# Optimization experiments

Measured on AMD Instinct MI355X. Metric: run time of the kernel, lower is better.

Reference implementation:

```python
import jax, jax.numpy as jnp
import numpy as np

D_MODEL, D_CTX, D_HEAD = 1024, 768, 16

def setup_inputs() -> dict:
    key = jax.random.key(0)
    ks = jax.random.split(key, 10)
    B, M, N = 8, 4096, 4096
    s = lambda d: 1.0 / np.sqrt(d)
    return {
        "x": jax.random.normal(ks[0], (B, M, D_MODEL), dtype=jnp.float32),
        "context": jax.random.normal(ks[1], (B, N, D_CTX), dtype=jnp.float32),
        "Wq": jax.random.uniform(ks[2], (D_MODEL, D_HEAD), jnp.float32, -s(D_MODEL), s(D_MODEL)),
        "bq": jax.random.uniform(ks[3], (D_HEAD,), jnp.float32, -s(D_MODEL), s(D_MODEL)),
        "Wk": jax.random.uniform(ks[4], (D_CTX, D_HEAD), jnp.float32, -s(D_CTX), s(D_CTX)),
        "bk": jax.random.uniform(ks[5], (D_HEAD,), jnp.float32, -s(D_CTX), s(D_CTX)),
        "Wv": jax.random.uniform(ks[6], (D_CTX, D_HEAD), jnp.float32, -s(D_CTX), s(D_CTX)),
        "bv": jax.random.uniform(ks[7], (D_HEAD,), jnp.float32, -s(D_CTX), s(D_CTX)),
        "Wo": jax.random.uniform(ks[8], (D_HEAD, D_MODEL), jnp.float32, -s(D_HEAD), s(D_HEAD)),
        "bo": jax.random.uniform(ks[9], (D_MODEL,), jnp.float32, -s(D_HEAD), s(D_HEAD)),
    }

def _kernel(t):
    # ELU+1 feature map (non-negative)
    return jax.nn.elu(t) + 1.0

def reference(x, context, Wq, bq, Wk, bk, Wv, bv, Wo, bo):
    Q = _kernel(x @ Wq + bq)            # (B, M, d_head)
    K = _kernel(context @ Wk + bk)      # (B, N, d_head)
    V = context @ Wv + bv               # (B, N, d_head)
    KtV = jnp.einsum('bnd,bne->bde', K, V)   # (B, d_head, d_head)
    num = jnp.einsum('bmd,bde->bme', Q, KtV) # (B, M, d_head)
    K_sum = K.sum(axis=1)                    # (B, d_head)
    denom = jnp.einsum('bmd,bd->bm', Q, K_sum)[..., None] + 1e-6
    out = num / denom                        # (B, M, d_head)
    return out @ Wo + bo                     # (B, M, d_model)
```

## Files before the change

### kernel.cpp

```cpp
#include <hip/hip_runtime.h>
#include <math.h>

#define B_   8
#define M_   4096
#define N_   4096
#define DM   1024
#define DC   768
#define DH   16
#define PD   8
#define KVBLOCKS (B_*N_/32)
#define CHUNKS   128

typedef float v4f __attribute__((ext_vector_type(4)));
typedef __attribute__((ext_vector_type(8))) short short8v;
typedef __attribute__((ext_vector_type(4))) float f32x4;
typedef __attribute__((ext_vector_type(4))) int int4v;

__device__ __forceinline__ float elu1(float t) {
    return t > 0.0f ? t + 1.0f : expf(t);
}
__device__ __forceinline__ float4 ld4(const float* p) { return *reinterpret_cast<const float4*>(p); }
__device__ __forceinline__ void  st4(float* p, float4 v) { *reinterpret_cast<float4*>(p) = v; }
__device__ __forceinline__ void  st4nt(float* p, float4 v) {
    v4f w; w.x = v.x; w.y = v.y; w.z = v.z; w.w = v.w;
    __builtin_nontemporal_store(w, reinterpret_cast<v4f*>(p));
}
__device__ __forceinline__ void fma4(float4& a, float s, float4 w) {
    a.x = fmaf(s, w.x, a.x); a.y = fmaf(s, w.y, a.y);
    a.z = fmaf(s, w.z, a.z); a.w = fmaf(s, w.w, a.w);
}
__device__ __forceinline__ short f2bf(float f) {
    unsigned u = __float_as_uint(f);
    unsigned r = 0x7FFFu + ((u >> 16) & 1u);
    return (short)((u + r) >> 16);
}
__device__ __forceinline__ unsigned cvtpk(float a, float b) {
    unsigned r;
    asm("v_cvt_pk_bf16_f32 %0, %1, %2" : "=v"(r) : "v"(a), "v"(b));
    return r;
}
__device__ __forceinline__ short8v mk_frag(const float4& a, const float4& b) {
    int4v iv;
    iv.x = (int)cvtpk(a.x, a.y);
    iv.y = (int)cvtpk(a.z, a.w);
    iv.z = (int)cvtpk(b.x, b.y);
    iv.w = (int)cvtpk(b.z, b.w);
    union { int4v i; short8v s; } u; u.i = iv;
    return u.s;
}

__global__ __launch_bounds__(256) void prep(
    const float* __restrict__ Wq, const float* __restrict__ Wk,
    const float* __restrict__ Wv,
    short* __restrict__ fq, short* __restrict__ fk, short* __restrict__ fv)
{
    const int id = blockIdx.x * 256 + threadIdx.x;
    if (id >= 80 * 64) return;
    const int l  = id & 63;
    const int kt = id >> 6;
    const float* W; short* dst; int ktl;
    if (kt < 32)      { W = Wq; dst = fq; ktl = kt; }
    else if (kt < 56) { W = Wk; dst = fk; ktl = kt - 32; }
    else              { W = Wv; dst = fv; ktl = kt - 56; }
    const int k0 = ktl * 32 + (l >> 4) * 8;
    const int d  = l & 15;
    short* o = dst + ((size_t)ktl * 64 + l) * 8;
    #pragma unroll
    for (int j = 0; j < 8; ++j)
        o[j] = f2bf(W[(size_t)(k0 + j) * DH + d]);
}

__global__ __launch_bounds__(256) void kvr(
    const float* __restrict__ ctx,
    const short* __restrict__ fk, const short* __restrict__ fv,
    const float* __restrict__ bk, const float* __restrict__ bv,
    float* __restrict__ part)
{
    __shared__ struct {
        float ka[2][2][16][17];
        float va[2][2][16][17];
        float sk[32][17];
        float sv[32][17];
    } sh;

    const int t  = threadIdx.x;
    const int l  = t & 63;
    const int w  = t >> 6;
    const int rt = w & 1;
    const int kh = w >> 1;
    const int g4 = l >> 4;
    const int lr = l & 15;

    float4 pa[PD], pb[PD];
    const size_t row0 = (size_t)blockIdx.x * 32;
    const float* src = ctx + (row0 + rt*16 + lr) * DC + kh*384 + g4*8;
    f32x4 accK = {0,0,0,0}, accV = {0,0,0,0};

    #pragma unroll
    for (int i = 0; i < PD; ++i) {
        pa[i] = ld4(src + i*32);
        pb[i] = ld4(src + i*32 + 4);
    }
    #pragma unroll
    for (int kt = 0; kt < 12; ++kt) {
        const int st = kt & (PD-1);
        const short8v a = mk_frag(pa[st], pb[st]);
        if (kt + PD < 12) {
            pa[st] = ld4(src + (kt+PD)*32);
            pb[st] = ld4(src + (kt+PD)*32 + 4);
        }
        const int ktg = kh*12 + kt;
        const short8v bkf = *reinterpret_cast<const short8v*>(fk + ((size_t)ktg*64 + l)*8);
        const short8v bvf = *reinterpret_cast<const short8v*>(fv + ((size_t)ktg*64 + l)*8);
        accK = __builtin_amdgcn_mfma_f32_16x16x32_bf16(a, bkf, accK, 0, 0, 0);
        accV = __builtin_amdgcn_mfma_f32_16x16x32_bf16(a, bvf, accV, 0, 0, 0);
    }

    #pragma unroll
    for (int j = 0; j < 4; ++j) {
        sh.ka[rt][kh][g4*4 + j][lr] = accK[j];
        sh.va[rt][kh][g4*4 + j][lr] = accV[j];
    }
    __syncthreads();

    #pragma unroll
    for (int i = t; i < 512; i += 256) {
        const int r = i >> 4, c = i & 15;
        const int rr = r >> 4, wr = r & 15;
        const float kk = sh.ka[rr][0][wr][c] + sh.ka[rr][1][wr][c] + bk[c];
        const float vv = sh.va[rr][0][wr][c] + sh.va[rr][1][wr][c] + bv[c];
        sh.sk[r][c] = elu1(kk);
        sh.sv[r][c] = vv;
    }
    __syncthreads();

    const int d = t >> 4, e = t & 15;
    float acc = 0.f;
    #pragma unroll 16
    for (int n = 0; n < 32; ++n) acc += sh.sk[n][d] * sh.sv[n][e];
    float* p = part + (size_t)blockIdx.x * 272;
    p[t] = acc;
    if (t < DH) {
        float ss = 0.f;
        #pragma unroll 16
        for (int n = 0; n < 32; ++n) ss += sh.sk[n][t];
        p[256 + t] = ss;
    }
}

__global__ __launch_bounds__(320) void reduce2(
    const float* __restrict__ part, float* __restrict__ comb)
{
    const int b = blockIdx.x;
    const int t = threadIdx.x;
    if (t < 272) {
        float s = 0.f;
        #pragma unroll
        for (int ch = 0; ch < CHUNKS; ++ch)
            s += part[((size_t)b*CHUNKS + ch) * 272 + t];
        comb[(size_t)b*272 + t] = s;
    }
}

__global__ __launch_bounds__(256) void qproj(
    const float* __restrict__ x,
    const short* __restrict__ fq, const float* __restrict__ bq,
    const float* __restrict__ comb,
    const float* __restrict__ Wo, const float* __restrict__ bo,
    float* __restrict__ out)
{
    __shared__ float qa[4][16][17];
    __shared__ float ql[16 * DH];
    __shared__ float ol[16 * DH];
    __shared__ float kts[272];

    const int t  = threadIdx.x;
    const int l  = t & 63;
    const int w  = t >> 6;
    const int g4 = l >> 4;
    const int lr = l & 15;
    const size_t row0 = (size_t)blockIdx.x * 16;
    const int b = blockIdx.x >> 8;

    const float* src = x + (row0 + lr) * DM + w*256 + g4*8;
    float4 pa[8], pb[8];
    #pragma unroll
    for (int i = 0; i < 8; ++i) {
        pa[i] = ld4(src + i*32);
        pb[i] = ld4(src + i*32 + 4);
    }
    if (t < 68) st4(&kts[t*4], ld4(comb + (size_t)b*272 + t*4));

    f32x4 accQ = {0,0,0,0};
    #pragma unroll
    for (int kt = 0; kt < 8; ++kt) {
        const short8v a = mk_frag(pa[kt], pb[kt]);
        const short8v bqf = *reinterpret_cast<const short8v*>(fq + ((size_t)(w*8 + kt)*64 + l)*8);
        accQ = __builtin_amdgcn_mfma_f32_16x16x32_bf16(a, bqf, accQ, 0, 0, 0);
    }
    #pragma unroll
    for (int j = 0; j < 4; ++j)
        qa[w][g4*4 + j][lr] = accQ[j];
    __syncthreads();

    {
        const int r = t >> 4, c = t & 15;
        const float v = qa[0][r][c] + qa[1][r][c] + qa[2][r][c] + qa[3][r][c] + bq[c];
        ql[r*DH + c] = elu1(v);
    }
    __syncthreads();

    if (t < 64) {
        const float* qrow = &ql[(t >> 2) * DH];
        const int jj = (t & 3) * 4;
        float den = 1e-6f;
        float4 num = make_float4(0,0,0,0);
        #pragma unroll
        for (int d4 = 0; d4 < 4; ++d4) {
            const float4 q4  = ld4(&qrow[d4*4]);
            const float4 ks4 = ld4(&kts[256 + d4*4]);
            den += q4.x*ks4.x + q4.y*ks4.y + q4.z*ks4.z + q4.w*ks4.w;
            fma4(num, q4.x, ld4(&kts[(d4*4+0)*DH + jj]));
            fma4(num, q4.y, ld4(&kts[(d4*4+1)*DH + jj]));
            fma4(num, q4.z, ld4(&kts[(d4*4+2)*DH + jj]));
            fma4(num, q4.w, ld4(&kts[(d4*4+3)*DH + jj]));
        }
        const float inv = 1.0f / den;
        float4 o4; o4.x = num.x*inv; o4.y = num.y*inv; o4.z = num.z*inv; o4.w = num.w*inv;
        st4(&ol[(t >> 2)*DH + jj], o4);
    }
    __syncthreads();

    float4 wreg[16];
    #pragma unroll
    for (int e = 0; e < 16; ++e) wreg[e] = ld4(Wo + (size_t)e*DM + t*4);
    const float4 bov = ld4(bo + t*4);

    #pragma unroll
    for (int r = 0; r < 16; ++r) {
        float4 a = bov;
        #pragma unroll
        for (int eo = 0; eo < 4; ++eo) {
            const float4 o4 = ld4(&ol[r*DH + eo*4]);
            fma4(a, o4.x, wreg[eo*4+0]); fma4(a, o4.y, wreg[eo*4+1]);
            fma4(a, o4.z, wreg[eo*4+2]); fma4(a, o4.w, wreg[eo*4+3]);
        }
        st4nt(out + (row0 + r)*DM + t*4, a);
    }
}

extern "C" void kernel_launch(void* const* d_in, const int* in_sizes, int n_in,
                              void* d_out, int out_size, void* d_ws, size_t ws_size,
                              hipStream_t stream) {
    const float* x    = (const float*)d_in[0];
    const float* ctx  = (const float*)d_in[1];
    const float* Wq   = (const float*)d_in[2];
    const float* bq   = (const float*)d_in[3];
    const float* Wk   = (const float*)d_in[4];
    const float* bk   = (const float*)d_in[5];
    const float* Wv   = (const float*)d_in[6];
    const float* bv   = (const float*)d_in[7];
    const float* Wo   = (const float*)d_in[8];
    const float* bo   = (const float*)d_in[9];
    float* out = (float*)d_out;

    float* ws = (float*)d_ws;
    float* part = ws;
    float* comb = part + (size_t)KVBLOCKS*272;
    short* fq = (short*)(comb + (size_t)B_*272);
    short* fk = fq + (size_t)32*64*8;
    short* fv = fk + (size_t)24*64*8;

    prep<<<dim3(20), dim3(256), 0, stream>>>(Wq, Wk, Wv, fq, fk, fv);
    kvr<<<dim3(KVBLOCKS), dim3(256), 0, stream>>>(ctx, fk, fv, bk, bv, part);
    reduce2<<<dim3(B_), dim3(320), 0, stream>>>(part, comb);
    qproj<<<dim3(B_*M_/16), dim3(256), 0, stream>>>(x, fq, bq, comb, Wo, bo, out);
}
```

Measured before the change: 73.49 us.

## Replace KV partial-sum reduction kernel with atomics and enlarge Q-projection row tiles

The kvr kernel now atomically accumulates its per-block KtV and K-sum partials into a zeroed per-batch buffer, so the separate reduce2 launch and the partials array go away. The qproj kernel processes 32 rows per block instead of 16. Its waves split into row-tile and K-half pairs with a register-prefetched K loop, halving the block count and amortising the Wo register load. Costs are 272 atomic adds per kvr block into only 8 small regions, a memset launch, and non-deterministic float summation order.

```diff
diff --git a/kernel.cpp b/kernel.cpp
--- a/kernel.cpp
+++ b/kernel.cpp
@@ -9,7 +9,7 @@
 #define DH   16
 #define PD   8
 #define KVBLOCKS (B_*N_/32)
-#define CHUNKS   128
+#define QBLOCKS  (B_*M_/32)
 
 typedef float v4f __attribute__((ext_vector_type(4)));
 typedef __attribute__((ext_vector_type(8))) short short8v;
@@ -74,7 +74,7 @@
     const float* __restrict__ ctx,
     const short* __restrict__ fk, const short* __restrict__ fv,
     const float* __restrict__ bk, const float* __restrict__ bv,
-    float* __restrict__ part)
+    float* __restrict__ comb)
 {
     __shared__ struct {
         float ka[2][2][16][17];
@@ -138,27 +138,13 @@
     float acc = 0.f;
     #pragma unroll 16
     for (int n = 0; n < 32; ++n) acc += sh.sk[n][d] * sh.sv[n][e];
-    float* p = part + (size_t)blockIdx.x * 272;
-    p[t] = acc;
+    float* p = comb + (size_t)(blockIdx.x >> 7) * 272;
+    atomicAdd(&p[t], acc);
     if (t < DH) {
         float ss = 0.f;
         #pragma unroll 16
         for (int n = 0; n < 32; ++n) ss += sh.sk[n][t];
-        p[256 + t] = ss;
-    }
-}
-
-__global__ __launch_bounds__(320) void reduce2(
-    const float* __restrict__ part, float* __restrict__ comb)
-{
-    const int b = blockIdx.x;
-    const int t = threadIdx.x;
-    if (t < 272) {
-        float s = 0.f;
-        #pragma unroll
-        for (int ch = 0; ch < CHUNKS; ++ch)
-            s += part[((size_t)b*CHUNKS + ch) * 272 + t];
-        comb[(size_t)b*272 + t] = s;
+        atomicAdd(&p[256 + t], ss);
     }
 }
 
@@ -169,23 +155,25 @@
     const float* __restrict__ Wo, const float* __restrict__ bo,
     float* __restrict__ out)
 {
-    __shared__ float qa[4][16][17];
-    __shared__ float ql[16 * DH];
-    __shared__ float ol[16 * DH];
+    __shared__ float qa[2][2][16][17];
+    __shared__ float ql[32 * DH];
+    __shared__ float ol[32 * DH];
     __shared__ float kts[272];
 
     const int t  = threadIdx.x;
     const int l  = t & 63;
     const int w  = t >> 6;
+    const int rt = w & 1;
+    const int kh = w >> 1;
     const int g4 = l >> 4;
     const int lr = l & 15;
-    const size_t row0 = (size_t)blockIdx.x * 16;
-    const int b = blockIdx.x >> 8;
-
-    const float* src = x + (row0 + lr) * DM + w*256 + g4*8;
-    float4 pa[8], pb[8];
-    #pragma unroll
-    for (int i = 0; i < 8; ++i) {
+    const size_t row0 = (size_t)blockIdx.x * 32;
+    const int b = blockIdx.x >> 7;
+
+    const float* src = x + (row0 + rt*16 + lr) * DM + kh*512 + g4*8;
+    float4 pa[PD], pb[PD];
+    #pragma unroll
+    for (int i = 0; i < PD; ++i) {
         pa[i] = ld4(src + i*32);
         pb[i] = ld4(src + i*32 + 4);
     }
@@ -193,24 +181,32 @@
 
     f32x4 accQ = {0,0,0,0};
     #pragma unroll
-    for (int kt = 0; kt < 8; ++kt) {
-        const short8v a = mk_frag(pa[kt], pb[kt]);
-        const short8v bqf = *reinterpret_cast<const short8v*>(fq + ((size_t)(w*8 + kt)*64 + l)*8);
+    for (int kt = 0; kt < 16; ++kt) {
+        const int st = kt & (PD-1);
+        const short8v a = mk_frag(pa[st], pb[st]);
+        if (kt + PD < 16) {
+            pa[st] = ld4(src + (kt+PD)*32);
+            pb[st] = ld4(src + (kt+PD)*32 + 4);
+        }
+        const int ktg = kh*16 + kt;
+        const short8v bqf = *reinterpret_cast<const short8v*>(fq + ((size_t)ktg*64 + l)*8);
         accQ = __builtin_amdgcn_mfma_f32_16x16x32_bf16(a, bqf, accQ, 0, 0, 0);
     }
     #pragma unroll
     for (int j = 0; j < 4; ++j)
-        qa[w][g4*4 + j][lr] = accQ[j];
-    __syncthreads();
-
-    {
-        const int r = t >> 4, c = t & 15;
-        const float v = qa[0][r][c] + qa[1][r][c] + qa[2][r][c] + qa[3][r][c] + bq[c];
+        qa[rt][kh][g4*4 + j][lr] = accQ[j];
+    __syncthreads();
+
+    #pragma unroll
+    for (int i = t; i < 512; i += 256) {
+        const int r = i >> 4, c = i & 15;
+        const int rr = r >> 4, wr = r & 15;
+        const float v = qa[rr][0][wr][c] + qa[rr][1][wr][c] + bq[c];
         ql[r*DH + c] = elu1(v);
     }
     __syncthreads();
 
-    if (t < 64) {
+    if (t < 128) {
         const float* qrow = &ql[(t >> 2) * DH];
         const int jj = (t & 3) * 4;
         float den = 1e-6f;
@@ -236,8 +232,8 @@
     for (int e = 0; e < 16; ++e) wreg[e] = ld4(Wo + (size_t)e*DM + t*4);
     const float4 bov = ld4(bo + t*4);
 
-    #pragma unroll
-    for (int r = 0; r < 16; ++r) {
+    #pragma unroll 4
+    for (int r = 0; r < 32; ++r) {
         float4 a = bov;
         #pragma unroll
         for (int eo = 0; eo < 4; ++eo) {
@@ -265,14 +261,13 @@
     float* out = (float*)d_out;
 
     float* ws = (float*)d_ws;
-    float* part = ws;
-    float* comb = part + (size_t)KVBLOCKS*272;
+    float* comb = ws;
     short* fq = (short*)(comb + (size_t)B_*272);
     short* fk = fq + (size_t)32*64*8;
     short* fv = fk + (size_t)24*64*8;
 
+    hipMemsetAsync(comb, 0, (size_t)B_*272*sizeof(float), stream);
     prep<<<dim3(20), dim3(256), 0, stream>>>(Wq, Wk, Wv, fq, fk, fv);
-    kvr<<<dim3(KVBLOCKS), dim3(256), 0, stream>>>(ctx, fk, fv, bk, bv, part);
-    reduce2<<<dim3(B_), dim3(320), 0, stream>>>(part, comb);
-    qproj<<<dim3(B_*M_/16), dim3(256), 0, stream>>>(x, fq, bq, comb, Wo, bo, out);
-}
+    kvr<<<dim3(KVBLOCKS), dim3(256), 0, stream>>>(ctx, fk, fv, bk, bv, comb);
+    qproj<<<dim3(QBLOCKS), dim3(256), 0, stream>>>(x, fq, bq, comb, Wo, bo, out);
+}
```

New measurement: 74.72 us. No clear change (+1.7%).
